# Kernel tuning notes

Measured on AMD Instinct MI355X. Metric: run time of the kernel, lower is better.

## Reference

```python
import jax, jax.numpy as jnp
import numpy as np

N, CIN, T, V = 64, 192, 256, 25
K, COUT, S = 3, 64, 5  # kernel_size, out_channels, num_semantic


def setup_inputs() -> dict:
    key = jax.random.key(0)
    ks = jax.random.split(key, 8)
    x = jax.random.normal(ks[0], (N, CIN, T, V), jnp.float32)
    A = jax.random.normal(ks[1], (K, V, V), jnp.float32)
    node_type = jnp.arange(V, dtype=jnp.int64) % S  # every semantic type present
    Wc = jax.random.normal(ks[2], (COUT * K, CIN), jnp.float32) * 0.02
    bc = jax.random.normal(ks[3], (COUT * K,), jnp.float32) * 0.02
    W1 = jax.random.normal(ks[4], (S * COUT, COUT * K), jnp.float32) * 0.02
    b1 = jax.random.normal(ks[5], (S * COUT,), jnp.float32) * 0.02
    W2 = jax.random.normal(ks[6], (S * COUT, COUT * K), jnp.float32) * 0.02
    b2 = jax.random.normal(ks[7], (S * COUT,), jnp.float32) * 0.02
    return {"x": x, "A": A, "node_type": node_type, "Wc": Wc, "bc": bc,
            "W1": W1, "b1": b1, "W2": W2, "b2": b2}


def reference(x, A, node_type, Wc, bc, W1, b1, W2, b2):
    # self.conv: 1x1 conv (t_kernel_size=1) -> (N, K*COUT, T, V)
    y = jnp.einsum('nctv,oc->notv', x, Wc) + bc[None, :, None, None]
    # conv1 / conv2 applied to tmp_x = y, reshape to (N, S, COUT, T, V), mean over T
    x1 = (jnp.einsum('nctv,oc->notv', y, W1) + b1[None, :, None, None]).reshape(N, S, COUT, T, V)
    x2 = (jnp.einsum('nctv,oc->notv', y, W2) + b2[None, :, None, None]).reshape(N, S, COUT, T, V)
    x1 = x1.mean(axis=3, keepdims=True)  # (N, S, COUT, 1, V)
    x2 = x2.mean(axis=3, keepdims=True)  # (N, S, COUT, 1, V)
    # per-semantic masked mean over nodes (vectorized over the 5 semantic types)
    masks = (node_type[None, :] == jnp.arange(S)[:, None]).astype(y.dtype)  # (S, V)
    counts = masks.sum(axis=-1)  # (S,)
    sem = jnp.einsum('nsclv,sv->nscl', x1, masks) / counts[None, :, None, None]  # (N,S,COUT,1)
    # diff: (N, S, COUT, 1, 1, V)  (graph_list stacked over the semantic axis)
    graphs = sem[..., None, None] - x2[:, :, :, :, None, :]
    # graph conv with adjacency A
    xk = y.reshape(N, K, COUT, T, V)
    out = jnp.einsum('nkctv,kvw->nctw', xk, A)  # (N, COUT, T, V)
    return out, A, graphs
```

## Files before the change

kernel.cpp:

```cpp
#include <hip/hip_runtime.h>

#define N_    64
#define CIN_  192
#define T_    256
#define V_    25
#define K_    3
#define COUT_ 64
#define OC_   192
#define SS_   5

#define OUT_OFF_A (N_*COUT_*T_*V_)
#define OUT_OFF_G (OUT_OFF_A + K_*V_*V_)

#define TCH   2
#define HCH   8
#define NCOLS 50
#define NCT   4
#define XB_STRIDE 200
#define XB_ROWS 64
#define XB_SH  (XB_ROWS*XB_STRIDE)
#define YB_STRIDE 104
#define YB_ROWS 128
#define YB_OFF  (2*XB_SH)
#define U_SHORTS (YB_OFF + YB_ROWS*YB_STRIDE)
#define NYV  4800
#define CPN  (T_/(TCH*HCH))
#define NBLK (N_*CPN)
#define SUNITS (25*(CIN_/8))
#define UPT 3

typedef __attribute__((ext_vector_type(8))) short short8;
typedef __attribute__((ext_vector_type(4))) float float4v;

__device__ inline unsigned bf16r(float f) {
    unsigned u = __float_as_uint(f);
    return (u + 0x7fffu + ((u >> 16) & 1u)) >> 16;
}

__global__ __launch_bounds__(256) void prep(const float* __restrict__ Wc,
                                            const float* __restrict__ A,
                                            short* __restrict__ WcB,
                                            short* __restrict__ A2T,
                                            float* __restrict__ out) {
    int idx = blockIdx.x * 256 + threadIdx.x;
    if (idx < OC_ * CIN_) WcB[idx] = (short)bf16r(Wc[idx]);
    if (idx < 32 * YB_STRIDE) {
        int w = idx / YB_STRIDE, kk = idx - w * YB_STRIDE;
        short val = 0;
        if (w < V_ && kk < K_ * V_) {
            int k = kk / V_, v = kk - k * V_;
            val = (short)bf16r(A[k * V_ * V_ + v * V_ + w]);
        }
        A2T[idx] = val;
    }
    if (idx < K_ * V_ * V_) out[OUT_OFF_A + idx] = A[idx];
}

__global__ __launch_bounds__(256, 2) void fused_mfma(const float* __restrict__ x,
                                                     const short* __restrict__ WcB,
                                                     const float* __restrict__ bc,
                                                     const short* __restrict__ A2T,
                                                     float* __restrict__ out,
                                                     float* __restrict__ part) {
    __shared__ __align__(16) short U[U_SHORTS];

    const int tid  = threadIdx.x;
    const int lane = tid & 63;
    const int wv   = tid >> 6;
    const int l15  = lane & 15;
    const int q    = lane >> 4;
    const int n    = blockIdx.x >> 4;
    const int tc   = blockIdx.x & 15;
    const int rt0  = wv * 3;

    {
        int4 z = make_int4(0, 0, 0, 0);
        for (int i = tid; i < U_SHORTS / 8; i += 256) ((int4*)U)[i] = z;
    }
    __syncthreads();

    short8 wfrag[3][6];
    {
        const short* wb = WcB + (rt0 * 16 + l15) * CIN_ + q * 8;
#pragma unroll
        for (int j = 0; j < 3; ++j)
#pragma unroll
            for (int ks = 0; ks < 6; ++ks)
                wfrag[j][ks] = *(const short8*)(wb + j * 16 * CIN_ + ks * 32);
    }
    float4v bvec[3];
#pragma unroll
    for (int j = 0; j < 3; ++j)
        bvec[j] = *(const float4v*)(bc + (rt0 + j) * 16 + q * 4);

    float racc[19];
#pragma unroll
    for (int u = 0; u < 19; ++u) racc[u] = 0.f;

    const float* xn = x + (size_t)n * (CIN_ * T_ * V_);
    const int tbase = tc * (TCH * HCH);

    for (int u = tid; u < SUNITS; u += 256) {
        int col2 = u % 25, cg = u / 25;
        const float* xp = xn + (size_t)(cg * 8) * (T_ * V_) + tbase * V_ + col2 * 2;
        short8 a, b;
#pragma unroll
        for (int j = 0; j < 8; ++j) {
            float2 f = *(const float2*)(xp + (size_t)j * (T_ * V_));
            a[j] = (short)bf16r(f.x);
            b[j] = (short)bf16r(f.y);
        }
        *(short8*)&U[(col2 * 2 + 0) * XB_STRIDE + cg * 8] = a;
        *(short8*)&U[(col2 * 2 + 1) * XB_STRIDE + cg * 8] = b;
    }

    for (int h = 0; h < HCH; ++h) {
        const int bs = (h & 1) * XB_SH;
        const int ob = ((h & 1) ^ 1) * XB_SH;
        const int t0 = tbase + h * TCH;
        const bool stage_ok = (h < HCH - 1);

        __syncthreads();

        float2 tmp[UPT][8];
#pragma unroll
        for (int s = 0; s < UPT; ++s) {
            int u = tid + s * 256;
            if (stage_ok && u < SUNITS) {
                int col2 = u % 25, cg = u / 25;
                const float* xp = xn + (size_t)(cg * 8) * (T_ * V_) + (t0 + TCH) * V_ + col2 * 2;
#pragma unroll
                for (int j = 0; j < 8; ++j)
                    tmp[s][j] = *(const float2*)(xp + (size_t)j * (T_ * V_));
            }
        }

        float4v acc[3][NCT];
#pragma unroll
        for (int j = 0; j < 3; ++j)
#pragma unroll
            for (int ct = 0; ct < NCT; ++ct) acc[j][ct] = bvec[j];

#pragma unroll
        for (int ct = 0; ct < NCT; ++ct) {
            const short* xb = &U[bs + (ct * 16 + l15) * XB_STRIDE + q * 8];
#pragma unroll
            for (int ks = 0; ks < 6; ++ks) {
                short8 bfrag = *(const short8*)(xb + ks * 32);
#pragma unroll
                for (int j = 0; j < 3; ++j)
                    acc[j][ct] = __builtin_amdgcn_mfma_f32_16x16x32_bf16(
                        wfrag[j][ks], bfrag, acc[j][ct], 0, 0, 0);
            }
        }

#pragma unroll
        for (int ct = 0; ct < NCT; ++ct) {
            int col = ct * 16 + l15;
            if (col < NCOLS) {
                int tl = col / V_;
                int v  = col - tl * V_;
#pragma unroll
                for (int j = 0; j < 3; ++j) {
                    int obase = (rt0 + j) * 16 + q * 4;
#pragma unroll
                    for (int i = 0; i < 4; ++i) {
                        int o   = obase + i;
                        int row = tl * 64 + (o & 63);
                        int cY  = (o >> 6) * V_ + v;
                        U[YB_OFF + row * YB_STRIDE + cY] = (short)bf16r(acc[j][ct][i]);
                    }
                }
            }
        }
        __syncthreads();

        short8 b2[2][3];
#pragma unroll
        for (int nt = 0; nt < 2; ++nt)
#pragma unroll
            for (int ks = 0; ks < 3; ++ks)
                b2[nt][ks] = *(const short8*)&A2T[(nt * 16 + l15) * YB_STRIDE + ks * 32 + q * 8];

        float4v o2[2][2];
#pragma unroll
        for (int mt = 0; mt < 2; ++mt)
#pragma unroll
            for (int nt = 0; nt < 2; ++nt) o2[mt][nt] = (float4v){0.f, 0.f, 0.f, 0.f};

#pragma unroll
        for (int mt = 0; mt < 2; ++mt) {
            int m = (wv * 2 + mt) * 16 + l15;
            const short* yb = &U[YB_OFF + m * YB_STRIDE + q * 8];
#pragma unroll
            for (int ks = 0; ks < 3; ++ks) {
                short8 af = *(const short8*)(yb + ks * 32);
#pragma unroll
                for (int nt = 0; nt < 2; ++nt)
                    o2[mt][nt] = __builtin_amdgcn_mfma_f32_16x16x32_bf16(
                        af, b2[nt][ks], o2[mt][nt], 0, 0, 0);
            }
        }

#pragma unroll
        for (int mt = 0; mt < 2; ++mt) {
#pragma unroll
            for (int nt = 0; nt < 2; ++nt) {
                int w = nt * 16 + l15;
                if (w < V_) {
#pragma unroll
                    for (int i = 0; i < 4; ++i) {
                        int m  = (wv * 2 + mt) * 16 + q * 4 + i;
                        int cc = m & 63, tl = m >> 6;
                        out[((size_t)(n * COUT_ + cc) * T_ + (t0 + tl)) * V_ + w] = o2[mt][nt][i];
                    }
                }
            }
        }

#pragma unroll
        for (int u = 0; u < 19; ++u) {
            int idx = tid + u * 256;
            if (u < 18 || idx < NYV) {
                int o = idx / V_, v = idx - (idx / V_) * V_;
                int cc = o & 63, k = o >> 6;
                const short* yp = &U[YB_OFF + cc * YB_STRIDE + k * V_ + v];
                float s = 0.f;
#pragma unroll
                for (int tl = 0; tl < TCH; ++tl) {
                    unsigned b = (unsigned short)yp[tl * 64 * YB_STRIDE];
                    s += __uint_as_float(b << 16);
                }
                racc[u] += s;
            }
        }

        if (stage_ok) {
#pragma unroll
            for (int s = 0; s < UPT; ++s) {
                int u = tid + s * 256;
                if (u < SUNITS) {
                    int col2 = u % 25, cg = u / 25;
                    short8 a, b;
#pragma unroll
                    for (int j = 0; j < 8; ++j) {
                        a[j] = (short)bf16r(tmp[s][j].x);
                        b[j] = (short)bf16r(tmp[s][j].y);
                    }
                    *(short8*)&U[ob + (col2 * 2 + 0) * XB_STRIDE + cg * 8] = a;
                    *(short8*)&U[ob + (col2 * 2 + 1) * XB_STRIDE + cg * 8] = b;
                }
            }
        }
    }

    float* pb = part + (size_t)blockIdx.x * NYV;
#pragma unroll
    for (int u = 0; u < 19; ++u) {
        int idx = tid + u * 256;
        if (u < 18 || idx < NYV) pb[idx] = racc[u];
    }
}

__global__ __launch_bounds__(256) void yred(const float* __restrict__ part,
                                            float* __restrict__ ysum) {
    int i = blockIdx.x * 256 + threadIdx.x;
    if (i >= N_ * NYV) return;
    int n = i / NYV;
    int r = i - n * NYV;
    const float* p = part + (size_t)n * CPN * NYV + r;
    float s = 0.f;
#pragma unroll
    for (int tc = 0; tc < CPN; ++tc) s += p[tc * NYV];
    ysum[i] = s * (1.0f / T_);
}

__global__ __launch_bounds__(256) void e2_graphs(const float* __restrict__ ysum,
                                                 const float* __restrict__ W1,
                                                 const float* __restrict__ b1,
                                                 const float* __restrict__ W2,
                                                 const float* __restrict__ b2,
                                                 const int* __restrict__ node_type,
                                                 float* __restrict__ out) {
    __shared__ float s1[10][V_];
    __shared__ float sem[10];
    const int tid = threadIdx.x;
    const int n  = blockIdx.x >> 5;
    const int jc = blockIdx.x & 31;
    const int jl = tid / V_;
    const int v  = tid - jl * V_;
    const int j  = jc * 10 + jl;
    float x2 = 0.f;
    if (jl < 10) {
        const float* yb = ysum + (size_t)n * NYV + v;
        const float* w1 = W1 + j * OC_;
        const float* w2 = W2 + j * OC_;
        float a1 = b1[j], a2 = b2[j];
        for (int o = 0; o < OC_; ++o) {
            float yv = yb[o * V_];
            a1 += w1[o] * yv;
            a2 += w2[o] * yv;
        }
        s1[jl][v] = a1;
        x2 = a2;
    }
    __syncthreads();
    if (tid < 10) {
        int s = (jc * 10 + tid) >> 6;
        float sum = 0.f, cnt = 0.f;
        for (int vv = 0; vv < V_; ++vv)
            if (node_type[vv] == s) { sum += s1[tid][vv]; cnt += 1.f; }
        sem[tid] = sum / cnt;
    }
    __syncthreads();
    if (jl < 10)
        out[OUT_OFF_G + (size_t)n * (SS_ * COUT_ * V_) + j * V_ + v] = sem[jl] - x2;
}

extern "C" void kernel_launch(void* const* d_in, const int* in_sizes, int n_in,
                              void* d_out, int out_size, void* d_ws, size_t ws_size,
                              hipStream_t stream) {
    const float* x         = (const float*)d_in[0];
    const float* A         = (const float*)d_in[1];
    const int*   node_type = (const int*)d_in[2];
    const float* Wc        = (const float*)d_in[3];
    const float* bc        = (const float*)d_in[4];
    const float* W1        = (const float*)d_in[5];
    const float* b1        = (const float*)d_in[6];
    const float* W2        = (const float*)d_in[7];
    const float* b2        = (const float*)d_in[8];
    float* out = (float*)d_out;

    float* part = (float*)d_ws;
    float* ysum = part + (size_t)NBLK * NYV;
    short* WcB  = (short*)(ysum + N_ * NYV);
    short* A2T  = WcB + OC_ * CIN_;

    hipLaunchKernelGGL(prep, dim3((OC_ * CIN_ + 255) / 256), dim3(256), 0, stream,
                       Wc, A, WcB, A2T, out);
    hipLaunchKernelGGL(fused_mfma, dim3(NBLK), dim3(256), 0, stream,
                       x, WcB, bc, A2T, out, part);
    hipLaunchKernelGGL(yred, dim3((N_ * NYV + 255) / 256), dim3(256), 0, stream,
                       part, ysum);
    hipLaunchKernelGGL(e2_graphs, dim3(N_ * 32), dim3(256), 0, stream,
                       ysum, W1, b1, W2, b2, node_type, out);
}
```

Baseline: 636.8 us.

## Replace partial-sum reduction kernel with atomics, single-buffer X tile, longer time chunks

Each block now covers twice as many time steps, so there are half as many blocks. Blocks add their per-sample Y sums straight into a zeroed ysum buffer with atomicAdd, and the separate yred kernel and its large partial buffer are removed. The 1/T scaling moves into e2_graphs. The X staging buffer in LDS goes from double to single buffering, which shrinks the shared memory footprint, and the A2T fragment load is hoisted out of the time loop. The aim is to cut global memory traffic and one kernel launch. In exchange there is atomic contention, float summation order becomes nondeterministic, and fewer blocks may lower parallelism.

```diff
diff --git a/kernel.cpp b/kernel.cpp
--- a/kernel.cpp
+++ b/kernel.cpp
@@ -13,7 +13,7 @@
 #define OUT_OFF_G (OUT_OFF_A + K_*V_*V_)
 
 #define TCH   2
-#define HCH   8
+#define HCH   16
 #define NCOLS 50
 #define NCT   4
 #define XB_STRIDE 200
@@ -21,7 +21,7 @@
 #define XB_SH  (XB_ROWS*XB_STRIDE)
 #define YB_STRIDE 104
 #define YB_ROWS 128
-#define YB_OFF  (2*XB_SH)
+#define YB_OFF  XB_SH
 #define U_SHORTS (YB_OFF + YB_ROWS*YB_STRIDE)
 #define NYV  4800
 #define CPN  (T_/(TCH*HCH))
@@ -41,6 +41,7 @@
                                             const float* __restrict__ A,
                                             short* __restrict__ WcB,
                                             short* __restrict__ A2T,
+                                            float* __restrict__ ysum,
                                             float* __restrict__ out) {
     int idx = blockIdx.x * 256 + threadIdx.x;
     if (idx < OC_ * CIN_) WcB[idx] = (short)bf16r(Wc[idx]);
@@ -54,6 +55,7 @@
         A2T[idx] = val;
     }
     if (idx < K_ * V_ * V_) out[OUT_OFF_A + idx] = A[idx];
+    if (idx < N_ * NYV) ysum[idx] = 0.f;
 }
 
 __global__ __launch_bounds__(256, 2) void fused_mfma(const float* __restrict__ x,
@@ -61,7 +63,7 @@
                                                      const float* __restrict__ bc,
                                                      const short* __restrict__ A2T,
                                                      float* __restrict__ out,
-                                                     float* __restrict__ part) {
+                                                     float* __restrict__ ysum) {
     __shared__ __align__(16) short U[U_SHORTS];
 
     const int tid  = threadIdx.x;
@@ -69,8 +71,8 @@
     const int wv   = tid >> 6;
     const int l15  = lane & 15;
     const int q    = lane >> 4;
-    const int n    = blockIdx.x >> 4;
-    const int tc   = blockIdx.x & 15;
+    const int n    = blockIdx.x >> 3;
+    const int tc   = blockIdx.x & 7;
     const int rt0  = wv * 3;
 
     {
@@ -92,6 +94,13 @@
 #pragma unroll
     for (int j = 0; j < 3; ++j)
         bvec[j] = *(const float4v*)(bc + (rt0 + j) * 16 + q * 4);
+
+    short8 b2[2][3];
+#pragma unroll
+    for (int nt = 0; nt < 2; ++nt)
+#pragma unroll
+        for (int ks = 0; ks < 3; ++ks)
+            b2[nt][ks] = *(const short8*)&A2T[(nt * 16 + l15) * YB_STRIDE + ks * 32 + q * 8];
 
     float racc[19];
 #pragma unroll
@@ -115,8 +124,6 @@
     }
 
     for (int h = 0; h < HCH; ++h) {
-        const int bs = (h & 1) * XB_SH;
-        const int ob = ((h & 1) ^ 1) * XB_SH;
         const int t0 = tbase + h * TCH;
         const bool stage_ok = (h < HCH - 1);
 
@@ -143,7 +150,7 @@
 
 #pragma unroll
         for (int ct = 0; ct < NCT; ++ct) {
-            const short* xb = &U[bs + (ct * 16 + l15) * XB_STRIDE + q * 8];
+            const short* xb = &U[(ct * 16 + l15) * XB_STRIDE + q * 8];
 #pragma unroll
             for (int ks = 0; ks < 6; ++ks) {
                 short8 bfrag = *(const short8*)(xb + ks * 32);
@@ -175,13 +182,6 @@
         }
         __syncthreads();
 
-        short8 b2[2][3];
-#pragma unroll
-        for (int nt = 0; nt < 2; ++nt)
-#pragma unroll
-            for (int ks = 0; ks < 3; ++ks)
-                b2[nt][ks] = *(const short8*)&A2T[(nt * 16 + l15) * YB_STRIDE + ks * 32 + q * 8];
-
         float4v o2[2][2];
 #pragma unroll
         for (int mt = 0; mt < 2; ++mt)
@@ -247,32 +247,19 @@
                         a[j] = (short)bf16r(tmp[s][j].x);
                         b[j] = (short)bf16r(tmp[s][j].y);
                     }
-                    *(short8*)&U[ob + (col2 * 2 + 0) * XB_STRIDE + cg * 8] = a;
-                    *(short8*)&U[ob + (col2 * 2 + 1) * XB_STRIDE + cg * 8] = b;
+                    *(short8*)&U[(col2 * 2 + 0) * XB_STRIDE + cg * 8] = a;
+                    *(short8*)&U[(col2 * 2 + 1) * XB_STRIDE + cg * 8] = b;
                 }
             }
         }
     }
 
-    float* pb = part + (size_t)blockIdx.x * NYV;
+    float* yb = ysum + (size_t)n * NYV;
 #pragma unroll
     for (int u = 0; u < 19; ++u) {
         int idx = tid + u * 256;
-        if (u < 18 || idx < NYV) pb[idx] = racc[u];
-    }
-}
-
-__global__ __launch_bounds__(256) void yred(const float* __restrict__ part,
-                                            float* __restrict__ ysum) {
-    int i = blockIdx.x * 256 + threadIdx.x;
-    if (i >= N_ * NYV) return;
-    int n = i / NYV;
-    int r = i - n * NYV;
-    const float* p = part + (size_t)n * CPN * NYV + r;
-    float s = 0.f;
-#pragma unroll
-    for (int tc = 0; tc < CPN; ++tc) s += p[tc * NYV];
-    ysum[i] = s * (1.0f / T_);
+        if (u < 18 || idx < NYV) atomicAdd(&yb[idx], racc[u]);
+    }
 }
 
 __global__ __launch_bounds__(256) void e2_graphs(const float* __restrict__ ysum,
@@ -295,14 +282,14 @@
         const float* yb = ysum + (size_t)n * NYV + v;
         const float* w1 = W1 + j * OC_;
         const float* w2 = W2 + j * OC_;
-        float a1 = b1[j], a2 = b2[j];
+        float a1 = 0.f, a2 = 0.f;
         for (int o = 0; o < OC_; ++o) {
             float yv = yb[o * V_];
             a1 += w1[o] * yv;
             a2 += w2[o] * yv;
         }
-        s1[jl][v] = a1;
-        x2 = a2;
+        s1[jl][v] = b1[j] + a1 * (1.0f / T_);
+        x2 = b2[j] + a2 * (1.0f / T_);
     }
     __syncthreads();
     if (tid < 10) {
@@ -331,17 +318,14 @@
     const float* b2        = (const float*)d_in[8];
     float* out = (float*)d_out;
 
-    float* part = (float*)d_ws;
-    float* ysum = part + (size_t)NBLK * NYV;
+    float* ysum = (float*)d_ws;
     short* WcB  = (short*)(ysum + N_ * NYV);
     short* A2T  = WcB + OC_ * CIN_;
 
-    hipLaunchKernelGGL(prep, dim3((OC_ * CIN_ + 255) / 256), dim3(256), 0, stream,
-                       Wc, A, WcB, A2T, out);
+    hipLaunchKernelGGL(prep, dim3((N_ * NYV + 255) / 256), dim3(256), 0, stream,
+                       Wc, A, WcB, A2T, ysum, out);
     hipLaunchKernelGGL(fused_mfma, dim3(NBLK), dim3(256), 0, stream,
-                       x, WcB, bc, A2T, out, part);
-    hipLaunchKernelGGL(yred, dim3((N_ * NYV + 255) / 256), dim3(256), 0, stream,
-                       part, ysum);
+                       x, WcB, bc, A2T, out, ysum);
     hipLaunchKernelGGL(e2_graphs, dim3(N_ * 32), dim3(256), 0, stream,
                        ysum, W1, b1, W2, b2, node_type, out);
 }
```

After: 618.8 us. 2.8% less time.
